# Kernel tuning notes

Measured on AMD Instinct MI355X. Metric: run time of the kernel, lower is better.

The kernel has to match this reference:

```python
import jax, jax.numpy as jnp
import numpy as np

B, SEQ, I_TSIZE, H, N_LAYERS = 512, 256, 64, 512, 2
E_CONST = 2.7183


def setup_inputs() -> dict:
    key = jax.random.key(0)
    ks = jax.random.split(key, 16)
    feats = jax.random.normal(ks[0], (B, SEQ, I_TSIZE - 1), dtype=jnp.float32)
    dt = jax.random.uniform(ks[1], (B, SEQ, 1), dtype=jnp.float32)  # elapsed time >= 0
    inputs_t = jnp.concatenate([feats, dt], axis=-1)  # [B, SEQ, I_TSIZE]
    i_size = I_TSIZE - 1
    inp = {"inputs_t": inputs_t}
    in_dims = [i_size, H]
    for l in range(N_LAYERS):
        c_inp = in_dims[l]
        s = 1.0 / np.sqrt(c_inp + H)
        inp[f"W{l}"] = jax.random.normal(ks[2 + 4 * l], (4 * H, c_inp + H), dtype=jnp.float32) * s
        inp[f"b{l}"] = jax.random.normal(ks[3 + 4 * l], (4 * H,), dtype=jnp.float32) * s
        sd = 1.0 / np.sqrt(H)
        inp[f"Wd{l}"] = jax.random.normal(ks[4 + 4 * l], (H, H), dtype=jnp.float32) * sd
        inp[f"bd{l}"] = jax.random.normal(ks[5 + 4 * l], (H,), dtype=jnp.float32) * sd
    return inp


def _tlstm_layer(curr_inp, W, b, Wd, bd):
    # curr_inp: [B, SEQ, feat+1] (last channel = dt). Scan over REVERSED time,
    # as in the torch loop `for t_seq in reversed(range(seq_l))`.
    batch = curr_inp.shape[0]
    h0 = jnp.zeros((batch, H), dtype=curr_inp.dtype)
    c0 = jnp.zeros((batch, H), dtype=curr_inp.dtype)

    def step(carry, xt):
        h, c = carry
        x, dt = xt[:, :-1], xt[:, -1:]
        T = 1.0 / jnp.log(dt + E_CONST)          # [B,1], broadcasts over H
        C_ST = jnp.tanh(h @ Wd.T + bd)
        h = h - C_ST + T * C_ST                  # time-decay correction
        z = jnp.concatenate([x, h], axis=1) @ W.T + b  # [B, 4H]
        ci, cf, co, cg = jnp.split(z, 4, axis=1)
        c_next = jax.nn.sigmoid(cf) * c + jax.nn.sigmoid(ci) * jnp.tanh(cg)
        h_next = jax.nn.sigmoid(co) * jnp.tanh(c_next)
        return (h_next, c_next), h_next

    xs = jnp.swapaxes(curr_inp[:, ::-1, :], 0, 1)  # [SEQ, B, feat+1], reversed time
    (h, c), hs = jax.lax.scan(step, (h0, c0), xs)
    # hs is in reversed-time order, matching torch's stack of output_inner
    layer_out = jnp.swapaxes(hs, 0, 1)  # [B, SEQ, H]
    return h, layer_out


def reference(inputs_t, W0, b0, Wd0, bd0, W1, b1, Wd1, bd1):
    t = inputs_t[..., -1:]  # [B, SEQ, 1], forward time order (as in torch code)
    params = [(W0, b0, Wd0, bd0), (W1, b1, Wd1, bd1)]
    curr = inputs_t
    h = None
    for (W, b, Wd, bd) in params:
        h, layer_out = _tlstm_layer(curr, W, b, Wd, bd)
        # NOTE: layer_out is in reversed time order but t is forward order;
        # this faithfully reproduces the original module's concatenation.
        curr = jnp.concatenate([layer_out, t], axis=-1)
    return h
```

## Files before the change

### kernel.cpp

```cpp
#include <hip/hip_runtime.h>
#include <stdint.h>

#define B_    512
#define SEQ_  256
#define H_    512
#define NSEQH (SEQ_ * H_)
#define NBLK  256
#define NTHR  (NBLK * 256)

using f32x4 = __attribute__((ext_vector_type(4))) float;
using s16x8 = __attribute__((ext_vector_type(8))) short;

#define WAITVM(N) asm volatile("s_waitcnt vmcnt(" #N ")" ::: "memory")
#define SBAR()    asm volatile("s_barrier" ::: "memory")

__device__ inline unsigned short f2bf(float f) {
  union { float f; uint32_t u; } x; x.f = f;
  uint32_t u = x.u;
  uint32_t r = u + 0x7fffu + ((u >> 16) & 1u);
  return (unsigned short)(r >> 16);
}
__device__ inline float bf2f(unsigned short h) {
  union { float f; uint32_t u; } x; x.u = ((uint32_t)h) << 16;
  return x.f;
}
__device__ inline float h2f(unsigned short u) {
  _Float16 h; __builtin_memcpy(&h, &u, 2); return (float)h;
}
__device__ inline unsigned short f2h(float f) {
  _Float16 h = (_Float16)f; unsigned short u; __builtin_memcpy(&u, &h, 2); return u;
}
__device__ inline float sigf(float x) { return 1.0f / (1.0f + expf(-x)); }

__device__ inline void gload16(const void* g, void* l) {
  __builtin_amdgcn_global_load_lds(
      (const __attribute__((address_space(1))) void*)g,
      (__attribute__((address_space(3))) void*)l, 16, 0, 0);
}
__device__ inline void gload16c(const void* g, void* l) {
  __builtin_amdgcn_global_load_lds(
      (const __attribute__((address_space(1))) void*)g,
      (__attribute__((address_space(3))) void*)l, 16, 0, 17);
}

__device__ __forceinline__ unsigned short ldh_coh(const unsigned short* p) {
  return __hip_atomic_load(p, __ATOMIC_RELAXED, __HIP_MEMORY_SCOPE_SYSTEM);
}
__device__ __forceinline__ void sth_coh(short* p, unsigned short v) {
  __hip_atomic_store((unsigned short*)p, v, __ATOMIC_RELAXED, __HIP_MEMORY_SCOPE_SYSTEM);
}

__device__ __forceinline__ void gbar_heavy(unsigned* bar) {
  __syncthreads();
  if (threadIdx.x == 0) {
    unsigned g = __hip_atomic_load(bar + 1, __ATOMIC_RELAXED, __HIP_MEMORY_SCOPE_AGENT);
    unsigned a = __hip_atomic_fetch_add(bar, 1u, __ATOMIC_ACQ_REL, __HIP_MEMORY_SCOPE_AGENT);
    if (a == (unsigned)(NBLK - 1)) {
      __hip_atomic_store(bar, 0u, __ATOMIC_RELAXED, __HIP_MEMORY_SCOPE_AGENT);
      __hip_atomic_store(bar + 1, g + 1u, __ATOMIC_RELEASE, __HIP_MEMORY_SCOPE_AGENT);
    } else {
      while (__hip_atomic_load(bar + 1, __ATOMIC_ACQUIRE, __HIP_MEMORY_SCOPE_AGENT) == g)
        __builtin_amdgcn_s_sleep(2);
    }
  }
  __syncthreads();
}

__device__ __forceinline__ void lbar(unsigned* bar, int& nb) {
  __syncthreads();
  ++nb;
  if (threadIdx.x == 0) {
    unsigned* leaf = bar + 32 + (blockIdx.x >> 5) * 32;
    unsigned* root = bar + 8;
    unsigned old = __hip_atomic_fetch_add(leaf, 1u, __ATOMIC_RELAXED, __HIP_MEMORY_SCOPE_SYSTEM);
    if ((old & 31u) == 31u)
      __hip_atomic_fetch_add(root, 1u, __ATOMIC_RELAXED, __HIP_MEMORY_SCOPE_SYSTEM);
    const unsigned target = (unsigned)(8 * nb);
    while ((int)(__hip_atomic_load(root, __ATOMIC_RELAXED, __HIP_MEMORY_SCOPE_SYSTEM) - target) < 0)
      __builtin_amdgcn_s_sleep(1);
  }
  __syncthreads();
}

__global__ void fill_kernel(float* __restrict__ out, int n, float v) {
  int i = blockIdx.x * blockDim.x + threadIdx.x;
  if (i < n) out[i] = v;
}

__device__ int compute_slot(const int* xcdmap, int myblk) {
  int cnt[8] = {0,0,0,0,0,0,0,0};
  int rank = -1;
  for (int b = 0; b < NBLK; ++b) {
    int x = xcdmap[b] & 7;
    int r = cnt[x]++;
    if (b == myblk) rank = r;
  }
  int myx = xcdmap[myblk] & 7;
  if (rank < 32) return myx * 32 + rank;
  int spill_idx = 0;
  {
    int c2[8] = {0,0,0,0,0,0,0,0};
    for (int b = 0; b < myblk; ++b) {
      int x = xcdmap[b] & 7;
      if (c2[x]++ >= 32) ++spill_idx;
    }
  }
  int k = 0;
  for (int g = 0; g < 8; ++g) {
    int filled = cnt[g] < 32 ? cnt[g] : 32;
    for (int rr = filled; rr < 32; ++rr) {
      if (k == spill_idx) return g * 32 + rr;
      ++k;
    }
  }
  return 0;
}

template<bool CVT>
__device__ __forceinline__ void g1_phase(
    char* LDS, int m0, int n0,
    const short* hhi, const short* hlo,
    const short* Wds, const float* bd, const float* tm1,
    short* huhi, short* hulo,
    const unsigned short* lo0_t, short* xhhi, short* xhlo)
{
  const int tid = threadIdx.x;
  const int w = tid >> 6, l = tid & 63;
  const int sr = tid >> 3;
  const int scs = (tid & 7) ^ (sr & 7);

  auto stage = [&](int kt) {
    char* base = LDS + (kt & 3) * 16384;
    const int kb = kt << 6;
    const size_t aoff = (size_t)(m0 + sr) * H_ + kb + scs * 8;
    gload16c(hhi + aoff, base + w * 1024);
    gload16c(hlo + aoff, base + 4096 + w * 1024);
    const size_t boff = (size_t)(n0 + sr) * 1024 + kb + scs * 8;
    gload16(Wds + boff,       base + 8192  + w * 1024);
    gload16(Wds + boff + 512, base + 12288 + w * 1024);
  };

  stage(0); stage(1); stage(2);

  const int wm = w & 1, wn = w >> 1;
  const int ar = wm * 16 + (l & 15);
  const int br = wn * 16 + (l & 15);
  const int koff = (l >> 4) * 16;
  const int aswz = (ar & 7) << 4;
  const int bswz = (br & 7) << 4;

  f32x4 acc = {0.f, 0.f, 0.f, 0.f};

  for (int kt = 0; kt < 8; ++kt) {
    if (kt < 6)       WAITVM(8);
    else if (kt == 6) WAITVM(4);
    else              WAITVM(0);
    SBAR();
    if (kt + 3 < 8) stage(kt + 3);
    char* base = LDS + (kt & 3) * 16384;
#pragma unroll
    for (int k2 = 0; k2 < 2; ++k2) {
      const int ao = (ar * 128 + k2 * 64 + koff) ^ aswz;
      const int bo = (br * 128 + k2 * 64 + koff) ^ bswz;
      s16x8 a_hi = *(const s16x8*)(base + ao);
      s16x8 a_lo = *(const s16x8*)(base + 4096 + ao);
      s16x8 b_hi = *(const s16x8*)(base + 8192 + bo);
      s16x8 b_lo = *(const s16x8*)(base + 12288 + bo);
      acc = __builtin_amdgcn_mfma_f32_16x16x32_bf16(a_hi, b_hi, acc, 0, 0, 0);
      acc = __builtin_amdgcn_mfma_f32_16x16x32_bf16(a_lo, b_hi, acc, 0, 0, 0);
      acc = __builtin_amdgcn_mfma_f32_16x16x32_bf16(a_hi, b_lo, acc, 0, 0, 0);
    }
  }

  const int n_abs = n0 + wn * 16 + (l & 15);
  const int mbase = m0 + wm * 16 + (l >> 4) * 4;
  const float bv = bd[n_abs];
#pragma unroll
  for (int r = 0; r < 4; ++r) {
    const int m_abs = mbase + r;
    const size_t off = (size_t)m_abs * H_ + n_abs;
    float cst = tanhf(acc[r] + bv);
    float hv = bf2f(ldh_coh((const unsigned short*)hhi + off)) +
               bf2f(ldh_coh((const unsigned short*)hlo + off));
    float hu = hv + tm1[m_abs] * cst;
    unsigned short hi = f2bf(hu);
    sth_coh(huhi + off, hi);
    sth_coh(hulo + off, f2bf(hu - bf2f(hi)));
    if (CVT) {
      float xv = h2f(ldh_coh(lo0_t + (size_t)m_abs * NSEQH + n_abs));
      unsigned short xh = f2bf(xv);
      sth_coh(xhhi + off, xh);
      sth_coh(xhlo + off, f2bf(xv - bf2f(xh)));
    }
  }
}

template<int K, int XK, int XSTR, bool STORE_LO0, bool XCOH>
__device__ __forceinline__ void g2_phase(
    char* LDS, int m0, int j0,
    const short* xhi, const short* xlo,
    const short* huhi, const short* hulo,
    const short* Wsp, const float* bias,
    f32x4& cv, short* hhi, short* hlo,
    unsigned short* lo0_t)
{
  constexpr int NT = K / 64;
  constexpr int KPS = 2 * K;
  const int tid = threadIdx.x;
  const int w = tid >> 6, l = tid & 63;

  auto stage = [&](int kt) {
    char* base = LDS + (kt & 1) * 32768;
    const int kb = kt << 6;
#pragma unroll
    for (int j = 0; j < 2; ++j) {
      const int s = tid + j * 256;
      const int r = s >> 3;
      const int cs = (s & 7) ^ (r & 7);
      const int dst = j * 4096 + w * 1024;
      if (kb < XK) {
        const size_t aoff = (size_t)(m0 + r) * XSTR + kb + cs * 8;
        if (XCOH) { gload16c(xhi + aoff, base + dst); gload16c(xlo + aoff, base + 8192 + dst); }
        else      { gload16 (xhi + aoff, base + dst); gload16 (xlo + aoff, base + 8192 + dst); }
      } else {
        const size_t aoff = (size_t)(m0 + r) * H_ + (kb - XK) + cs * 8;
        gload16c(huhi + aoff, base + dst);
        gload16c(hulo + aoff, base + 8192 + dst);
      }
      const int src_n = (r >> 4) * H_ + j0 + (r & 15);
      const size_t boff = (size_t)src_n * KPS + kb + cs * 8;
      gload16(Wsp + boff,     base + 16384 + dst);
      gload16(Wsp + boff + K, base + 24576 + dst);
    }
  };

  stage(0); stage(1);

  const int ar = w * 16 + (l & 15);
  const int koff = (l >> 4) * 16;
  const int aswz = (ar & 7) << 4;

  f32x4 acc[4];
#pragma unroll
  for (int i = 0; i < 4; ++i) acc[i] = (f32x4){0.f, 0.f, 0.f, 0.f};

  for (int kt = 0; kt < NT; ++kt) {
    if (kt + 1 < NT) WAITVM(8);
    else             WAITVM(0);
    SBAR();
    char* base = LDS + (kt & 1) * 32768;
#pragma unroll
    for (int k2 = 0; k2 < 2; ++k2) {
      const int ao = (ar * 128 + k2 * 64 + koff) ^ aswz;
      s16x8 a_hi = *(const s16x8*)(base + ao);
      s16x8 a_lo = *(const s16x8*)(base + 8192 + ao);
#pragma unroll
      for (int nf = 0; nf < 4; ++nf) {
        const int br = nf * 16 + (l & 15);
        const int bo = (br * 128 + k2 * 64 + koff) ^ ((br & 7) << 4);
        s16x8 b_hi = *(const s16x8*)(base + 16384 + bo);
        s16x8 b_lo = *(const s16x8*)(base + 24576 + bo);
        acc[nf] = __builtin_amdgcn_mfma_f32_16x16x32_bf16(a_hi, b_hi, acc[nf], 0, 0, 0);
        acc[nf] = __builtin_amdgcn_mfma_f32_16x16x32_bf16(a_lo, b_hi, acc[nf], 0, 0, 0);
        acc[nf] = __builtin_amdgcn_mfma_f32_16x16x32_bf16(a_hi, b_lo, acc[nf], 0, 0, 0);
      }
    }
    SBAR();
    if (kt + 2 < NT) stage(kt + 2);
  }

  const int j_abs = j0 + (l & 15);
  const float bi  = bias[j_abs];
  const float bfv = bias[H_ + j_abs];
  const float bo  = bias[2 * H_ + j_abs];
  const float bg  = bias[3 * H_ + j_abs];
  const int mbase = m0 + w * 16 + (l >> 4) * 4;
#pragma unroll
  for (int r = 0; r < 4; ++r) {
    const int m_abs = mbase + r;
    float zi = acc[0][r] + bi;
    float zf = acc[1][r] + bfv;
    float zo = acc[2][r] + bo;
    float zg = acc[3][r] + bg;
    float cn = sigf(zf) * cv[r] + sigf(zi) * tanhf(zg);
    float hn = sigf(zo) * tanhf(cn);
    cv[r] = cn;
    const size_t off = (size_t)m_abs * H_ + j_abs;
    unsigned short hi = f2bf(hn);
    sth_coh(hhi + off, hi);
    sth_coh(hlo + off, f2bf(hn - bf2f(hi)));
    if (STORE_LO0)
      sth_coh((short*)(lo0_t + (size_t)m_abs * NSEQH + j_abs), f2h(hn));
  }
}

__global__ __launch_bounds__(256, 1) void persist(
    const float* inputs,
    const float* W0, const float* b0, const float* Wd0, const float* bd0,
    const float* W1, const float* b1, const float* Wd1, const float* bd1,
    float* out,
    unsigned short* lo0, short* xinhi, short* xinlo,
    short* hhi, short* hlo, short* huhi, short* hulo,
    short* xhhi, short* xhlo,
    float* Tm1T, short* Wd0s, short* Wd1s, short* W0s, short* W1s,
    unsigned* bar, int* xcdmap)
{
  __shared__ __align__(16) char LDS[65536];
  const int gtid = blockIdx.x * 256 + threadIdx.x;
  int nb = 0;

  if (threadIdx.x == 0) {
    unsigned xcc;
    asm volatile("s_getreg_b32 %0, hwreg(20, 0, 32)" : "=s"(xcc));
    xcdmap[blockIdx.x] = (int)(xcc & 7u);
  }

  auto dosplit = [&](const float* W, short* Ws, int N, int Ksrc, int Kpad, int pad_at) {
    const int total = N * Kpad;
    for (int idx = gtid; idx < total; idx += NTHR) {
      int n = idx / Kpad, c = idx - n * Kpad;
      int sc = c;
      if (pad_at >= 0) { if (c == pad_at) sc = -1; else if (c > pad_at) sc = c - 1; }
      float v = 0.f;
      if (sc >= 0 && sc < Ksrc) v = W[(size_t)n * Ksrc + sc];
      unsigned short hi = f2bf(v);
      unsigned short lo = f2bf(v - bf2f(hi));
      size_t base = (size_t)n * (2 * Kpad);
      Ws[base + c]        = (short)hi;
      Ws[base + Kpad + c] = (short)lo;
    }
  };
  dosplit(Wd0, Wd0s, 512, 512, 512, -1);
  dosplit(Wd1, Wd1s, 512, 512, 512, -1);
  dosplit(W0, W0s, 2048, 575, 576, 63);
  dosplit(W1, W1s, 2048, 1024, 1024, -1);
  for (int idx = gtid; idx < B_ * SEQ_ * 64; idx += NTHR) {
    float v = inputs[idx];
    unsigned short hi = f2bf(v);
    xinhi[idx] = (short)hi;
    xinlo[idx] = (short)f2bf(v - bf2f(hi));
  }
  for (int idx = gtid; idx < B_ * SEQ_; idx += NTHR) {
    int b = idx / SEQ_, t = idx - b * SEQ_;
    float dt = inputs[(size_t)b * (SEQ_ * 64) + t * 64 + 63];
    Tm1T[t * B_ + b] = 1.0f / logf(dt + 2.7183f) - 1.0f;
  }
  for (int idx = gtid; idx < B_ * H_; idx += NTHR) {
    hhi[idx] = 0; hlo[idx] = 0;
  }
  gbar_heavy(bar);

  const int myw = compute_slot(xcdmap, blockIdx.x);
  const int wg = myw >> 5, rr = myw & 31;
  const int g1_n0 = (wg * 2 + (rr & 1)) * 32;
  const int g1_m0 = (rr >> 1) * 32;
  const int g2_j0 = (wg * 4 + (rr & 3)) * 16;
  const int g2_m0 = (rr >> 2) * 64;

  for (int layer = 0; layer < 2; ++layer) {
    f32x4 cv = {0.f, 0.f, 0.f, 0.f};
    if (layer == 1) {
      for (int idx = gtid; idx < B_ * H_; idx += NTHR) {
        sth_coh(hhi + idx, 0); sth_coh(hlo + idx, 0);
      }
      lbar(bar, nb);
    }
    for (int s = 0; s < SEQ_; ++s) {
      const int torig = SEQ_ - 1 - s;
      if (layer == 0) {
        g1_phase<false>(LDS, g1_m0, g1_n0, hhi, hlo, Wd0s, bd0,
                        Tm1T + (size_t)torig * B_, huhi, hulo,
                        nullptr, nullptr, nullptr);
        lbar(bar, nb);
        g2_phase<576, 64, SEQ_ * 64, true, false>(
            LDS, g2_m0, g2_j0,
            xinhi + (size_t)torig * 64, xinlo + (size_t)torig * 64,
            huhi, hulo, W0s, b0, cv, hhi, hlo,
            lo0 + (size_t)s * H_);
        lbar(bar, nb);
      } else {
        g1_phase<true>(LDS, g1_m0, g1_n0, hhi, hlo, Wd1s, bd1,
                       Tm1T + (size_t)torig * B_, huhi, hulo,
                       lo0 + (size_t)torig * H_, xhhi, xhlo);
        lbar(bar, nb);
        g2_phase<1024, 512, H_, false, true>(
            LDS, g2_m0, g2_j0,
            xhhi, xhlo, huhi, hulo, W1s, b1,
            cv, hhi, hlo, nullptr);
        lbar(bar, nb);
      }
    }
  }

  for (int idx = gtid; idx < B_ * H_; idx += NTHR)
    out[idx] = bf2f(ldh_coh((const unsigned short*)hhi + idx)) +
               bf2f(ldh_coh((const unsigned short*)hlo + idx));
}

extern "C" void kernel_launch(void* const* d_in, const int* in_sizes, int n_in,
                              void* d_out, int out_size, void* d_ws, size_t ws_size,
                              hipStream_t stream) {
  const float* inputs = (const float*)d_in[0];
  const float* W0  = (const float*)d_in[1];
  const float* b0  = (const float*)d_in[2];
  const float* Wd0 = (const float*)d_in[3];
  const float* bd0 = (const float*)d_in[4];
  const float* W1  = (const float*)d_in[5];
  const float* b1  = (const float*)d_in[6];
  const float* Wd1 = (const float*)d_in[7];
  const float* bd1 = (const float*)d_in[8];

  char* ws = (char*)d_ws;
  size_t off = 0;
  auto alloc = [&](size_t bytes) -> char* {
    char* p = ws + off;
    off += (bytes + 1023) & ~(size_t)1023;
    return p;
  };
  unsigned* bar = (unsigned*)alloc(2048);
  int* xcdmap = (int*)alloc(NBLK * 4);
  unsigned short* lo0 = (unsigned short*)alloc((size_t)B_ * SEQ_ * H_ * 2);
  short* xinhi = (short*)alloc((size_t)B_ * SEQ_ * 64 * 2);
  short* xinlo = (short*)alloc((size_t)B_ * SEQ_ * 64 * 2);
  short* hhi   = (short*)alloc((size_t)B_ * H_ * 2);
  short* hlo   = (short*)alloc((size_t)B_ * H_ * 2);
  short* huhi  = (short*)alloc((size_t)B_ * H_ * 2);
  short* hulo  = (short*)alloc((size_t)B_ * H_ * 2);
  short* xhhi  = (short*)alloc((size_t)B_ * H_ * 2);
  short* xhlo  = (short*)alloc((size_t)B_ * H_ * 2);
  float* Tm1T  = (float*)alloc((size_t)SEQ_ * B_ * 4);
  short* Wd0s  = (short*)alloc((size_t)512 * 1024 * 2);
  short* Wd1s  = (short*)alloc((size_t)512 * 1024 * 2);
  short* W0s   = (short*)alloc((size_t)2048 * 1152 * 2);
  short* W1s   = (short*)alloc((size_t)2048 * 2048 * 2);

  if (off > ws_size) {
    fill_kernel<<<(out_size + 255) / 256, 256, 0, stream>>>(
        (float*)d_out, out_size, (float)(ws_size >> 20));
    return;
  }

  hipMemsetAsync(bar, 0, 2048, stream);
  persist<<<NBLK, 256, 0, stream>>>(
      inputs, W0, b0, Wd0, bd0, W1, b1, Wd1, bd1,
      (float*)d_out,
      lo0, xinhi, xinlo,
      hhi, hlo, huhi, hulo, xhhi, xhlo,
      Tm1T, Wd0s, Wd1s, W0s, W1s, bar, xcdmap);
}
```

Baseline: 10.31 ms.

## Double persistent block count with half-size blocks and prime weight slices into L2

Runs the persistent kernel as 512 blocks of 128 threads instead of 256 blocks of 256. The XCD slot mapping, barrier targets, per-block GEMM tiles and LDS staging layouts are all rescaled to match. It also adds a prime pass in which one block per column slice reads its Wd and W weight slices so they are cached before the time loop. The goal is to spread the latency-bound recurrent steps over more CUs and warm the caches. The cost is a doubled barrier participant count, more blocks per CU, and extra startup reads.

After: 12.44 ms. 20.6% more time.

```diff
diff --git a/kernel.cpp b/kernel.cpp
--- a/kernel.cpp
+++ b/kernel.cpp
@@ -5,8 +5,9 @@
 #define SEQ_  256
 #define H_    512
 #define NSEQH (SEQ_ * H_)
-#define NBLK  256
-#define NTHR  (NBLK * 256)
+#define NBLK  512
+#define TPB   128
+#define NTHR  (NBLK * TPB)
 
 using f32x4 = __attribute__((ext_vector_type(4))) float;
 using s16x8 = __attribute__((ext_vector_type(8))) short;
@@ -75,7 +76,7 @@
     unsigned old = __hip_atomic_fetch_add(leaf, 1u, __ATOMIC_RELAXED, __HIP_MEMORY_SCOPE_SYSTEM);
     if ((old & 31u) == 31u)
       __hip_atomic_fetch_add(root, 1u, __ATOMIC_RELAXED, __HIP_MEMORY_SCOPE_SYSTEM);
-    const unsigned target = (unsigned)(8 * nb);
+    const unsigned target = (unsigned)(16 * nb);
     while ((int)(__hip_atomic_load(root, __ATOMIC_RELAXED, __HIP_MEMORY_SCOPE_SYSTEM) - target) < 0)
       __builtin_amdgcn_s_sleep(1);
   }
@@ -96,20 +97,20 @@
     if (b == myblk) rank = r;
   }
   int myx = xcdmap[myblk] & 7;
-  if (rank < 32) return myx * 32 + rank;
+  if (rank < 64) return myx * 64 + rank;
   int spill_idx = 0;
   {
     int c2[8] = {0,0,0,0,0,0,0,0};
     for (int b = 0; b < myblk; ++b) {
       int x = xcdmap[b] & 7;
-      if (c2[x]++ >= 32) ++spill_idx;
+      if (c2[x]++ >= 64) ++spill_idx;
     }
   }
   int k = 0;
   for (int g = 0; g < 8; ++g) {
-    int filled = cnt[g] < 32 ? cnt[g] : 32;
-    for (int rr = filled; rr < 32; ++rr) {
-      if (k == spill_idx) return g * 32 + rr;
+    int filled = cnt[g] < 64 ? cnt[g] : 64;
+    for (int rr = filled; rr < 64; ++rr) {
+      if (k == spill_idx) return g * 64 + rr;
       ++k;
     }
   }
@@ -126,25 +127,32 @@
 {
   const int tid = threadIdx.x;
   const int w = tid >> 6, l = tid & 63;
-  const int sr = tid >> 3;
-  const int scs = (tid & 7) ^ (sr & 7);
 
   auto stage = [&](int kt) {
-    char* base = LDS + (kt & 3) * 16384;
+    char* base = LDS + (kt & 3) * 12288;
     const int kb = kt << 6;
-    const size_t aoff = (size_t)(m0 + sr) * H_ + kb + scs * 8;
-    gload16c(hhi + aoff, base + w * 1024);
-    gload16c(hlo + aoff, base + 4096 + w * 1024);
-    const size_t boff = (size_t)(n0 + sr) * 1024 + kb + scs * 8;
-    gload16(Wds + boff,       base + 8192  + w * 1024);
-    gload16(Wds + boff + 512, base + 12288 + w * 1024);
+#pragma unroll
+    for (int j = 0; j < 2; ++j) {
+      const int s = tid + j * TPB;
+      const int r = s >> 3;
+      const int cs = (s & 7) ^ (r & 7);
+      const size_t aoff = (size_t)(m0 + r) * H_ + kb + cs * 8;
+      gload16c(hhi + aoff, base + j * 2048 + w * 1024);
+      gload16c(hlo + aoff, base + 4096 + j * 2048 + w * 1024);
+    }
+    {
+      const int r = tid >> 3;
+      const int cs = (tid & 7) ^ (r & 7);
+      const size_t boff = (size_t)(n0 + r) * 1024 + kb + cs * 8;
+      gload16(Wds + boff,       base + 8192  + w * 1024);
+      gload16(Wds + boff + 512, base + 10240 + w * 1024);
+    }
   };
 
   stage(0); stage(1); stage(2);
 
-  const int wm = w & 1, wn = w >> 1;
-  const int ar = wm * 16 + (l & 15);
-  const int br = wn * 16 + (l & 15);
+  const int ar = w * 16 + (l & 15);
+  const int br = l & 15;
   const int koff = (l >> 4) * 16;
   const int aswz = (ar & 7) << 4;
   const int bswz = (br & 7) << 4;
@@ -152,12 +160,12 @@
   f32x4 acc = {0.f, 0.f, 0.f, 0.f};
 
   for (int kt = 0; kt < 8; ++kt) {
-    if (kt < 6)       WAITVM(8);
-    else if (kt == 6) WAITVM(4);
+    if (kt < 6)       WAITVM(12);
+    else if (kt == 6) WAITVM(6);
     else              WAITVM(0);
     SBAR();
     if (kt + 3 < 8) stage(kt + 3);
-    char* base = LDS + (kt & 3) * 16384;
+    char* base = LDS + (kt & 3) * 12288;
 #pragma unroll
     for (int k2 = 0; k2 < 2; ++k2) {
       const int ao = (ar * 128 + k2 * 64 + koff) ^ aswz;
@@ -165,15 +173,15 @@
       s16x8 a_hi = *(const s16x8*)(base + ao);
       s16x8 a_lo = *(const s16x8*)(base + 4096 + ao);
       s16x8 b_hi = *(const s16x8*)(base + 8192 + bo);
-      s16x8 b_lo = *(const s16x8*)(base + 12288 + bo);
+      s16x8 b_lo = *(const s16x8*)(base + 10240 + bo);
       acc = __builtin_amdgcn_mfma_f32_16x16x32_bf16(a_hi, b_hi, acc, 0, 0, 0);
       acc = __builtin_amdgcn_mfma_f32_16x16x32_bf16(a_lo, b_hi, acc, 0, 0, 0);
       acc = __builtin_amdgcn_mfma_f32_16x16x32_bf16(a_hi, b_lo, acc, 0, 0, 0);
     }
   }
 
-  const int n_abs = n0 + wn * 16 + (l & 15);
-  const int mbase = m0 + wm * 16 + (l >> 4) * 4;
+  const int n_abs = n0 + (l & 15);
+  const int mbase = m0 + w * 16 + (l >> 4) * 4;
   const float bv = bd[n_abs];
 #pragma unroll
   for (int r = 0; r < 4; ++r) {
@@ -210,27 +218,34 @@
   const int w = tid >> 6, l = tid & 63;
 
   auto stage = [&](int kt) {
-    char* base = LDS + (kt & 1) * 32768;
+    char* base = LDS + (kt & 1) * 24576;
     const int kb = kt << 6;
 #pragma unroll
     for (int j = 0; j < 2; ++j) {
-      const int s = tid + j * 256;
+      const int s = tid + j * TPB;
       const int r = s >> 3;
       const int cs = (s & 7) ^ (r & 7);
-      const int dst = j * 4096 + w * 1024;
+      const int dst = j * 2048 + w * 1024;
       if (kb < XK) {
         const size_t aoff = (size_t)(m0 + r) * XSTR + kb + cs * 8;
-        if (XCOH) { gload16c(xhi + aoff, base + dst); gload16c(xlo + aoff, base + 8192 + dst); }
-        else      { gload16 (xhi + aoff, base + dst); gload16 (xlo + aoff, base + 8192 + dst); }
+        if (XCOH) { gload16c(xhi + aoff, base + dst); gload16c(xlo + aoff, base + 4096 + dst); }
+        else      { gload16 (xhi + aoff, base + dst); gload16 (xlo + aoff, base + 4096 + dst); }
       } else {
         const size_t aoff = (size_t)(m0 + r) * H_ + (kb - XK) + cs * 8;
         gload16c(huhi + aoff, base + dst);
-        gload16c(hulo + aoff, base + 8192 + dst);
+        gload16c(hulo + aoff, base + 4096 + dst);
       }
+    }
+#pragma unroll
+    for (int j = 0; j < 4; ++j) {
+      const int s = tid + j * TPB;
+      const int r = s >> 3;
+      const int cs = (s & 7) ^ (r & 7);
       const int src_n = (r >> 4) * H_ + j0 + (r & 15);
       const size_t boff = (size_t)src_n * KPS + kb + cs * 8;
-      gload16(Wsp + boff,     base + 16384 + dst);
-      gload16(Wsp + boff + K, base + 24576 + dst);
+      const int dst = 8192 + j * 2048 + w * 1024;
+      gload16(Wsp + boff,     base + dst);
+      gload16(Wsp + boff + K, base + 8192 + dst);
     }
   };
 
@@ -245,21 +260,21 @@
   for (int i = 0; i < 4; ++i) acc[i] = (f32x4){0.f, 0.f, 0.f, 0.f};
 
   for (int kt = 0; kt < NT; ++kt) {
-    if (kt + 1 < NT) WAITVM(8);
+    if (kt + 1 < NT) WAITVM(12);
     else             WAITVM(0);
     SBAR();
-    char* base = LDS + (kt & 1) * 32768;
+    char* base = LDS + (kt & 1) * 24576;
 #pragma unroll
     for (int k2 = 0; k2 < 2; ++k2) {
       const int ao = (ar * 128 + k2 * 64 + koff) ^ aswz;
       s16x8 a_hi = *(const s16x8*)(base + ao);
-      s16x8 a_lo = *(const s16x8*)(base + 8192 + ao);
+      s16x8 a_lo = *(const s16x8*)(base + 4096 + ao);
 #pragma unroll
       for (int nf = 0; nf < 4; ++nf) {
         const int br = nf * 16 + (l & 15);
         const int bo = (br * 128 + k2 * 64 + koff) ^ ((br & 7) << 4);
-        s16x8 b_hi = *(const s16x8*)(base + 16384 + bo);
-        s16x8 b_lo = *(const s16x8*)(base + 24576 + bo);
+        s16x8 b_hi = *(const s16x8*)(base + 8192 + bo);
+        s16x8 b_lo = *(const s16x8*)(base + 16384 + bo);
         acc[nf] = __builtin_amdgcn_mfma_f32_16x16x32_bf16(a_hi, b_hi, acc[nf], 0, 0, 0);
         acc[nf] = __builtin_amdgcn_mfma_f32_16x16x32_bf16(a_lo, b_hi, acc[nf], 0, 0, 0);
         acc[nf] = __builtin_amdgcn_mfma_f32_16x16x32_bf16(a_hi, b_lo, acc[nf], 0, 0, 0);
@@ -294,7 +309,7 @@
   }
 }
 
-__global__ __launch_bounds__(256, 1) void persist(
+__global__ __launch_bounds__(TPB, 1) void persist(
     const float* inputs,
     const float* W0, const float* b0, const float* Wd0, const float* bd0,
     const float* W1, const float* b1, const float* Wd1, const float* bd1,
@@ -303,10 +318,11 @@
     short* hhi, short* hlo, short* huhi, short* hulo,
     short* xhhi, short* xhlo,
     float* Tm1T, short* Wd0s, short* Wd1s, short* W0s, short* W1s,
-    unsigned* bar, int* xcdmap)
+    unsigned* bar, int* xcdmap, float* sink)
 {
-  __shared__ __align__(16) char LDS[65536];
-  const int gtid = blockIdx.x * 256 + threadIdx.x;
+  __shared__ __align__(16) char LDS[49152];
+  const int gtid = blockIdx.x * TPB + threadIdx.x;
+  const int tid = threadIdx.x;
   int nb = 0;
 
   if (threadIdx.x == 0) {
@@ -351,11 +367,26 @@
   gbar_heavy(bar);
 
   const int myw = compute_slot(xcdmap, blockIdx.x);
-  const int wg = myw >> 5, rr = myw & 31;
-  const int g1_n0 = (wg * 2 + (rr & 1)) * 32;
-  const int g1_m0 = (rr >> 1) * 32;
-  const int g2_j0 = (wg * 4 + (rr & 3)) * 16;
-  const int g2_m0 = (rr >> 2) * 64;
+  const int wg = myw >> 6, rr = myw & 63;
+  const int sl = wg * 4 + (rr & 3);
+  const int g1_n0 = sl * 16;
+  const int g1_m0 = (rr >> 2) * 32;
+  const int g2_j0 = sl * 16;
+  const int g2_m0 = (rr >> 2) * 32;
+
+  auto prime = [&](const short* p, int nshorts) {
+    float a = 0.f;
+    for (int i = tid * 8; i + 8 <= nshorts; i += TPB * 8) {
+      f32x4 v = *(const f32x4*)(p + i);
+      a += v[0] + v[1] + v[2] + v[3];
+    }
+    if (a == 1.0e38f) *sink = a;
+  };
+  if ((rr >> 2) == 0) {
+    prime(Wd0s + g1_n0 * 1024, 16 * 1024);
+    for (int g = 0; g < 4; ++g)
+      prime(W0s + (size_t)(g * 512 + g2_j0) * 2304, 16 * 2304);
+  }
 
   for (int layer = 0; layer < 2; ++layer) {
     f32x4 cv = {0.f, 0.f, 0.f, 0.f};
@@ -364,6 +395,11 @@
         sth_coh(hhi + idx, 0); sth_coh(hlo + idx, 0);
       }
       lbar(bar, nb);
+      if ((rr >> 2) == 0) {
+        prime(Wd1s + g1_n0 * 1024, 16 * 1024);
+        for (int g = 0; g < 4; ++g)
+          prime(W1s + (size_t)(g * 512 + g2_j0) * 4096, 16 * 4096);
+      }
     }
     for (int s = 0; s < SEQ_; ++s) {
       const int torig = SEQ_ - 1 - s;
@@ -417,8 +453,9 @@
     off += (bytes + 1023) & ~(size_t)1023;
     return p;
   };
-  unsigned* bar = (unsigned*)alloc(2048);
+  unsigned* bar = (unsigned*)alloc(4096);
   int* xcdmap = (int*)alloc(NBLK * 4);
+  float* sink = (float*)alloc(1024);
   unsigned short* lo0 = (unsigned short*)alloc((size_t)B_ * SEQ_ * H_ * 2);
   short* xinhi = (short*)alloc((size_t)B_ * SEQ_ * 64 * 2);
   short* xinlo = (short*)alloc((size_t)B_ * SEQ_ * 64 * 2);
@@ -440,11 +477,11 @@
     return;
   }
 
-  hipMemsetAsync(bar, 0, 2048, stream);
-  persist<<<NBLK, 256, 0, stream>>>(
+  hipMemsetAsync(bar, 0, 4096, stream);
+  persist<<<NBLK, TPB, 0, stream>>>(
       inputs, W0, b0, Wd0, bd0, W1, b1, Wd1, bd1,
       (float*)d_out,
       lo0, xinhi, xinlo,
       hhi, hlo, huhi, hulo, xhhi, xhlo,
-      Tm1T, Wd0s, Wd1s, W0s, W1s, bar, xcdmap);
-}
+      Tm1T, Wd0s, Wd1s, W0s, W1s, bar, xcdmap, sink);
+}
```

## Replace grid barriers with per-batch-tile flags and deepen GEMM pipelines

Applied to the files above, without the earlier changes.

Remaps work so that the g1 and g2 phases of each 64-row batch tile are owned by the same 32 blocks. The two grid-wide barriers per timestep become per-tile counter flags, so tiles advance independently and do not wait on the whole grid. The g2 GEMM moves from a double-buffered to a 4-stage LDS pipeline, dropping the second barrier per k-tile, and g1 is retiled. LDS is raised to 128KB of dynamic shared memory, which risks occupancy and adds the correctness burden of the new flag protocol.

Measured after the change: 16.43 ms. +59.4%, slower.

```diff
diff --git a/kernel.cpp b/kernel.cpp
--- a/kernel.cpp
+++ b/kernel.cpp
@@ -82,6 +82,20 @@
   __syncthreads();
 }
 
+__device__ __forceinline__ void flag_signal(unsigned* f) {
+  WAITVM(0);
+  __syncthreads();
+  if (threadIdx.x == 0)
+    __hip_atomic_fetch_add(f, 1u, __ATOMIC_RELAXED, __HIP_MEMORY_SCOPE_SYSTEM);
+}
+__device__ __forceinline__ void flag_wait(unsigned* f, unsigned target) {
+  if (threadIdx.x == 0 && target) {
+    while (__hip_atomic_load(f, __ATOMIC_RELAXED, __HIP_MEMORY_SCOPE_SYSTEM) < target)
+      __builtin_amdgcn_s_sleep(1);
+  }
+  __syncthreads();
+}
+
 __global__ void fill_kernel(float* __restrict__ out, int n, float v) {
   int i = blockIdx.x * blockDim.x + threadIdx.x;
   if (i < n) out[i] = v;
@@ -126,45 +140,48 @@
 {
   const int tid = threadIdx.x;
   const int w = tid >> 6, l = tid & 63;
-  const int sr = tid >> 3;
-  const int scs = (tid & 7) ^ (sr & 7);
+  const int ar_ = (tid & 127) >> 3;
+  const int acs = (tid & 7) ^ (ar_ & 7);
+  const short* Asel = (tid < 128) ? hhi : hlo;
+  const int adst = ((tid < 128) ? 0 : 2048) + (w & 1) * 1024;
 
   auto stage = [&](int kt) {
-    char* base = LDS + (kt & 3) * 16384;
+    char* base = LDS + (kt & 3) * 20480;
     const int kb = kt << 6;
-    const size_t aoff = (size_t)(m0 + sr) * H_ + kb + scs * 8;
-    gload16c(hhi + aoff, base + w * 1024);
-    gload16c(hlo + aoff, base + 4096 + w * 1024);
-    const size_t boff = (size_t)(n0 + sr) * 1024 + kb + scs * 8;
-    gload16(Wds + boff,       base + 8192  + w * 1024);
-    gload16(Wds + boff + 512, base + 12288 + w * 1024);
+    gload16c(Asel + (size_t)(m0 + ar_) * H_ + kb + acs * 8, base + adst);
+#pragma unroll
+    for (int q = 0; q < 4; ++q) {
+      const int r = ((q & 1) << 5) + w * 8 + (l >> 3);
+      const int cs = (l & 7) ^ (r & 7);
+      gload16(Wds + (size_t)(n0 + r) * 1024 + kb + ((q >> 1) ? 512 : 0) + cs * 8,
+              base + 4096 + (q >> 1) * 8192 + (q & 1) * 4096 + w * 1024);
+    }
   };
 
   stage(0); stage(1); stage(2);
 
-  const int wm = w & 1, wn = w >> 1;
-  const int ar = wm * 16 + (l & 15);
-  const int br = wn * 16 + (l & 15);
+  const int row_a = l & 15;
+  const int swz_a = (row_a & 7) << 4;
+  const int br = w * 16 + (l & 15);
+  const int swz_b = (br & 7) << 4;
   const int koff = (l >> 4) * 16;
-  const int aswz = (ar & 7) << 4;
-  const int bswz = (br & 7) << 4;
 
   f32x4 acc = {0.f, 0.f, 0.f, 0.f};
 
   for (int kt = 0; kt < 8; ++kt) {
-    if (kt < 6)       WAITVM(8);
-    else if (kt == 6) WAITVM(4);
+    if (kt < 6)       WAITVM(10);
+    else if (kt == 6) WAITVM(5);
     else              WAITVM(0);
     SBAR();
     if (kt + 3 < 8) stage(kt + 3);
-    char* base = LDS + (kt & 3) * 16384;
+    char* base = LDS + (kt & 3) * 20480;
 #pragma unroll
     for (int k2 = 0; k2 < 2; ++k2) {
-      const int ao = (ar * 128 + k2 * 64 + koff) ^ aswz;
-      const int bo = (br * 128 + k2 * 64 + koff) ^ bswz;
+      const int ao = (row_a * 128 + k2 * 64 + koff) ^ swz_a;
+      const int bo = (br * 128 + k2 * 64 + koff) ^ swz_b;
       s16x8 a_hi = *(const s16x8*)(base + ao);
-      s16x8 a_lo = *(const s16x8*)(base + 4096 + ao);
-      s16x8 b_hi = *(const s16x8*)(base + 8192 + bo);
+      s16x8 a_lo = *(const s16x8*)(base + 2048 + ao);
+      s16x8 b_hi = *(const s16x8*)(base + 4096 + bo);
       s16x8 b_lo = *(const s16x8*)(base + 12288 + bo);
       acc = __builtin_amdgcn_mfma_f32_16x16x32_bf16(a_hi, b_hi, acc, 0, 0, 0);
       acc = __builtin_amdgcn_mfma_f32_16x16x32_bf16(a_lo, b_hi, acc, 0, 0, 0);
@@ -172,8 +189,8 @@
     }
   }
 
-  const int n_abs = n0 + wn * 16 + (l & 15);
-  const int mbase = m0 + wm * 16 + (l >> 4) * 4;
+  const int n_abs = n0 + w * 16 + (l & 15);
+  const int mbase = m0 + (l >> 4) * 4;
   const float bv = bd[n_abs];
 #pragma unroll
   for (int r = 0; r < 4; ++r) {
@@ -210,48 +227,57 @@
   const int w = tid >> 6, l = tid & 63;
 
   auto stage = [&](int kt) {
-    char* base = LDS + (kt & 1) * 32768;
+    char* base = LDS + (kt & 3) * 32768;
     const int kb = kt << 6;
 #pragma unroll
-    for (int j = 0; j < 2; ++j) {
-      const int s = tid + j * 256;
-      const int r = s >> 3;
-      const int cs = (s & 7) ^ (r & 7);
-      const int dst = j * 4096 + w * 1024;
+    for (int q = 0; q < 4; ++q) {
+      const bool hi = q < 2;
+      const int qq = q & 1;
+      const int r = qq * 32 + w * 8 + (l >> 3);
+      const int cs = (l & 7) ^ (r & 7);
+      char* dst = base + (hi ? 0 : 8192) + qq * 4096 + w * 1024;
       if (kb < XK) {
+        const short* asrc = hi ? xhi : xlo;
         const size_t aoff = (size_t)(m0 + r) * XSTR + kb + cs * 8;
-        if (XCOH) { gload16c(xhi + aoff, base + dst); gload16c(xlo + aoff, base + 8192 + dst); }
-        else      { gload16 (xhi + aoff, base + dst); gload16 (xlo + aoff, base + 8192 + dst); }
+        if (XCOH) gload16c(asrc + aoff, dst);
+        else      gload16 (asrc + aoff, dst);
       } else {
-        const size_t aoff = (size_t)(m0 + r) * H_ + (kb - XK) + cs * 8;
-        gload16c(huhi + aoff, base + dst);
-        gload16c(hulo + aoff, base + 8192 + dst);
+        const short* asrc = hi ? huhi : hulo;
+        gload16c(asrc + (size_t)(m0 + r) * H_ + (kb - XK) + cs * 8, dst);
       }
+    }
+#pragma unroll
+    for (int q = 0; q < 4; ++q) {
+      const bool hi = q < 2;
+      const int qq = q & 1;
+      const int r = qq * 32 + w * 8 + (l >> 3);
+      const int cs = (l & 7) ^ (r & 7);
       const int src_n = (r >> 4) * H_ + j0 + (r & 15);
-      const size_t boff = (size_t)src_n * KPS + kb + cs * 8;
-      gload16(Wsp + boff,     base + 16384 + dst);
-      gload16(Wsp + boff + K, base + 24576 + dst);
+      gload16(Wsp + (size_t)src_n * KPS + kb + (hi ? 0 : K) + cs * 8,
+              base + 16384 + (hi ? 0 : 8192) + qq * 4096 + w * 1024);
     }
   };
 
-  stage(0); stage(1);
+  stage(0); stage(1); stage(2);
 
   const int ar = w * 16 + (l & 15);
+  const int swz_a = (ar & 7) << 4;
   const int koff = (l >> 4) * 16;
-  const int aswz = (ar & 7) << 4;
 
   f32x4 acc[4];
 #pragma unroll
   for (int i = 0; i < 4; ++i) acc[i] = (f32x4){0.f, 0.f, 0.f, 0.f};
 
   for (int kt = 0; kt < NT; ++kt) {
-    if (kt + 1 < NT) WAITVM(8);
-    else             WAITVM(0);
+    if (kt < NT - 2)       WAITVM(16);
+    else if (kt == NT - 2) WAITVM(8);
+    else                   WAITVM(0);
     SBAR();
-    char* base = LDS + (kt & 1) * 32768;
+    if (kt + 3 < NT) stage(kt + 3);
+    char* base = LDS + (kt & 3) * 32768;
 #pragma unroll
     for (int k2 = 0; k2 < 2; ++k2) {
-      const int ao = (ar * 128 + k2 * 64 + koff) ^ aswz;
+      const int ao = (ar * 128 + k2 * 64 + koff) ^ swz_a;
       s16x8 a_hi = *(const s16x8*)(base + ao);
       s16x8 a_lo = *(const s16x8*)(base + 8192 + ao);
 #pragma unroll
@@ -265,8 +291,6 @@
         acc[nf] = __builtin_amdgcn_mfma_f32_16x16x32_bf16(a_hi, b_lo, acc[nf], 0, 0, 0);
       }
     }
-    SBAR();
-    if (kt + 2 < NT) stage(kt + 2);
   }
 
   const int j_abs = j0 + (l & 15);
@@ -305,7 +329,7 @@
     float* Tm1T, short* Wd0s, short* Wd1s, short* W0s, short* W1s,
     unsigned* bar, int* xcdmap)
 {
-  __shared__ __align__(16) char LDS[65536];
+  extern __shared__ __align__(16) char LDS[];
   const int gtid = blockIdx.x * 256 + threadIdx.x;
   int nb = 0;
 
@@ -352,46 +376,54 @@
 
   const int myw = compute_slot(xcdmap, blockIdx.x);
   const int wg = myw >> 5, rr = myw & 31;
-  const int g1_n0 = (wg * 2 + (rr & 1)) * 32;
-  const int g1_m0 = (rr >> 1) * 32;
-  const int g2_j0 = (wg * 4 + (rr & 3)) * 16;
-  const int g2_m0 = (rr >> 2) * 64;
+  const int t = rr >> 2;
+  const int c = wg * 4 + (rr & 3);
+  const int g1_m0 = t * 64 + (c >> 3) * 16;
+  const int g1_n0 = (c & 7) * 64;
+  const int g2_m0 = t * 64;
+  const int g2_j0 = c * 16;
+  unsigned* g1d = bar + 512 + t * 16;
+  unsigned* g2d = bar + 768 + t * 16;
 
   for (int layer = 0; layer < 2; ++layer) {
     f32x4 cv = {0.f, 0.f, 0.f, 0.f};
     if (layer == 1) {
+      lbar(bar, nb);
       for (int idx = gtid; idx < B_ * H_; idx += NTHR) {
         sth_coh(hhi + idx, 0); sth_coh(hlo + idx, 0);
       }
       lbar(bar, nb);
     }
     for (int s = 0; s < SEQ_; ++s) {
+      const int ss = layer * SEQ_ + s;
       const int torig = SEQ_ - 1 - s;
-      if (layer == 0) {
+      flag_wait(g2d, 32u * (unsigned)ss);
+      if (layer == 0)
         g1_phase<false>(LDS, g1_m0, g1_n0, hhi, hlo, Wd0s, bd0,
                         Tm1T + (size_t)torig * B_, huhi, hulo,
                         nullptr, nullptr, nullptr);
-        lbar(bar, nb);
+      else
+        g1_phase<true>(LDS, g1_m0, g1_n0, hhi, hlo, Wd1s, bd1,
+                       Tm1T + (size_t)torig * B_, huhi, hulo,
+                       lo0 + (size_t)torig * H_, xhhi, xhlo);
+      flag_signal(g1d);
+      flag_wait(g1d, 32u * (unsigned)(ss + 1));
+      if (layer == 0)
         g2_phase<576, 64, SEQ_ * 64, true, false>(
             LDS, g2_m0, g2_j0,
             xinhi + (size_t)torig * 64, xinlo + (size_t)torig * 64,
             huhi, hulo, W0s, b0, cv, hhi, hlo,
             lo0 + (size_t)s * H_);
-        lbar(bar, nb);
-      } else {
-        g1_phase<true>(LDS, g1_m0, g1_n0, hhi, hlo, Wd1s, bd1,
-                       Tm1T + (size_t)torig * B_, huhi, hulo,
-                       lo0 + (size_t)torig * H_, xhhi, xhlo);
-        lbar(bar, nb);
+      else
         g2_phase<1024, 512, H_, false, true>(
             LDS, g2_m0, g2_j0,
             xhhi, xhlo, huhi, hulo, W1s, b1,
             cv, hhi, hlo, nullptr);
-        lbar(bar, nb);
-      }
-    }
-  }
-
+      flag_signal(g2d);
+    }
+  }
+
+  lbar(bar, nb);
   for (int idx = gtid; idx < B_ * H_; idx += NTHR)
     out[idx] = bf2f(ldh_coh((const unsigned short*)hhi + idx)) +
                bf2f(ldh_coh((const unsigned short*)hlo + idx));
@@ -417,7 +449,7 @@
     off += (bytes + 1023) & ~(size_t)1023;
     return p;
   };
-  unsigned* bar = (unsigned*)alloc(2048);
+  unsigned* bar = (unsigned*)alloc(4096);
   int* xcdmap = (int*)alloc(NBLK * 4);
   unsigned short* lo0 = (unsigned short*)alloc((size_t)B_ * SEQ_ * H_ * 2);
   short* xinhi = (short*)alloc((size_t)B_ * SEQ_ * 64 * 2);
@@ -440,8 +472,11 @@
     return;
   }
 
-  hipMemsetAsync(bar, 0, 2048, stream);
-  persist<<<NBLK, 256, 0, stream>>>(
+  hipFuncSetAttribute(reinterpret_cast<const void*>(&persist),
+                      hipFuncAttributeMaxDynamicSharedMemorySize, 131072);
+
+  hipMemsetAsync(bar, 0, 4096, stream);
+  persist<<<NBLK, 256, 131072, stream>>>(
       inputs, W0, b0, Wd0, bd0, W1, b1, Wd1, bd1,
       (float*)d_out,
       lo0, xinhi, xinlo,
```

## Load weights via registers and triple-buffer LDS in recurrent GEMM phases

Applied to the files above, without the earlier changes.

Weight tiles in both GEMM phases are now fetched into VGPRs with plain global loads and written to LDS one stage later, while activations still use direct global-to-LDS DMA. The LDS ring moves from 2–4 buffers to 3 buffers, backed by 96KB of dynamic shared memory. This lets the trailing barrier in g2 be dropped, so each K-step needs a single barrier and weight fetches overlap compute further ahead. In exchange it uses more registers and LDS, removes forceinline from both phases, and relies on exact waitcnt accounting that now also drains lgkmcnt.

After: 14.77 ms. +43.2%, slower.

```diff
diff --git a/kernel.cpp b/kernel.cpp
--- a/kernel.cpp
+++ b/kernel.cpp
@@ -11,7 +11,7 @@
 using f32x4 = __attribute__((ext_vector_type(4))) float;
 using s16x8 = __attribute__((ext_vector_type(8))) short;
 
-#define WAITVM(N) asm volatile("s_waitcnt vmcnt(" #N ")" ::: "memory")
+#define WAITVL(N) asm volatile("s_waitcnt vmcnt(" #N ") lgkmcnt(0)" ::: "memory")
 #define SBAR()    asm volatile("s_barrier" ::: "memory")
 
 __device__ inline unsigned short f2bf(float f) {
@@ -32,7 +32,7 @@
 }
 __device__ inline float sigf(float x) { return 1.0f / (1.0f + expf(-x)); }
 
-__device__ inline void gload16(const void* g, void* l) {
+__device__ inline void gldsw(const void* g, void* l) {
   __builtin_amdgcn_global_load_lds(
       (const __attribute__((address_space(1))) void*)g,
       (__attribute__((address_space(3))) void*)l, 16, 0, 0);
@@ -41,6 +41,11 @@
   __builtin_amdgcn_global_load_lds(
       (const __attribute__((address_space(1))) void*)g,
       (__attribute__((address_space(3))) void*)l, 16, 0, 17);
+}
+
+__device__ __forceinline__ void wload(const short* p, s16x8& d) {
+  asm volatile("global_load_dwordx4 %0, %1, off"
+               : "=&v"(d) : "v"((unsigned long long)p));
 }
 
 __device__ __forceinline__ unsigned short ldh_coh(const unsigned short* p) {
@@ -117,7 +122,7 @@
 }
 
 template<bool CVT>
-__device__ __forceinline__ void g1_phase(
+__device__ void g1_phase(
     char* LDS, int m0, int n0,
     const short* hhi, const short* hlo,
     const short* Wds, const float* bd, const float* tm1,
@@ -128,19 +133,33 @@
   const int w = tid >> 6, l = tid & 63;
   const int sr = tid >> 3;
   const int scs = (tid & 7) ^ (sr & 7);
-
-  auto stage = [&](int kt) {
-    char* base = LDS + (kt & 3) * 16384;
-    const int kb = kt << 6;
-    const size_t aoff = (size_t)(m0 + sr) * H_ + kb + scs * 8;
+  const int wc = tid & 7;
+  const int wdst = (sr * 128 + wc * 16) ^ ((sr & 7) << 4);
+
+  s16x8 vwh, vwl;
+  s16x8 twh, twl;
+
+  auto wloadW = [&](int kt, s16x8& a, s16x8& b) {
+    const short* p = Wds + (size_t)(n0 + sr) * 1024 + (kt << 6) + wc * 8;
+    wload(p, a); wload(p + 512, b);
+  };
+  auto dswriteW = [&](int kt, s16x8& a, s16x8& b) {
+    char* base = LDS + (kt % 3) * 16384;
+    *(s16x8*)(base + 8192 + wdst) = a;
+    *(s16x8*)(base + 12288 + wdst) = b;
+  };
+  auto admaA = [&](int kt) {
+    char* base = LDS + (kt % 3) * 16384;
+    const size_t aoff = (size_t)(m0 + sr) * H_ + (kt << 6) + scs * 8;
     gload16c(hhi + aoff, base + w * 1024);
     gload16c(hlo + aoff, base + 4096 + w * 1024);
-    const size_t boff = (size_t)(n0 + sr) * 1024 + kb + scs * 8;
-    gload16(Wds + boff,       base + 8192  + w * 1024);
-    gload16(Wds + boff + 512, base + 12288 + w * 1024);
-  };
-
-  stage(0); stage(1); stage(2);
+  };
+
+  wloadW(0, vwh, vwl); wloadW(1, twh, twl);
+  WAITVL(0);
+  dswriteW(0, vwh, vwl); dswriteW(1, twh, twl);
+  wloadW(2, vwh, vwl);
+  admaA(0); admaA(1);
 
   const int wm = w & 1, wn = w >> 1;
   const int ar = wm * 16 + (l & 15);
@@ -152,12 +171,13 @@
   f32x4 acc = {0.f, 0.f, 0.f, 0.f};
 
   for (int kt = 0; kt < 8; ++kt) {
-    if (kt < 6)       WAITVM(8);
-    else if (kt == 6) WAITVM(4);
-    else              WAITVM(0);
+    if (kt < 7) WAITVL(2);
+    else        WAITVL(0);
     SBAR();
-    if (kt + 3 < 8) stage(kt + 3);
-    char* base = LDS + (kt & 3) * 16384;
+    if (kt + 2 < 8) dswriteW(kt + 2, vwh, vwl);
+    if (kt + 3 < 8) wloadW(kt + 3, vwh, vwl);
+    if (kt + 2 < 8) admaA(kt + 2);
+    char* base = LDS + (kt % 3) * 16384;
 #pragma unroll
     for (int k2 = 0; k2 < 2; ++k2) {
       const int ao = (ar * 128 + k2 * 64 + koff) ^ aswz;
@@ -196,7 +216,7 @@
 }
 
 template<int K, int XK, int XSTR, bool STORE_LO0, bool XCOH>
-__device__ __forceinline__ void g2_phase(
+__device__ void g2_phase(
     char* LDS, int m0, int j0,
     const short* xhi, const short* xlo,
     const short* huhi, const short* hulo,
@@ -209,49 +229,77 @@
   const int tid = threadIdx.x;
   const int w = tid >> 6, l = tid & 63;
 
-  auto stage = [&](int kt) {
-    char* base = LDS + (kt & 1) * 32768;
+  const int wr0 = tid >> 3, wc0 = tid & 7;
+  const int wr1 = wr0 + 32;
+  const int wd0 = (wr0 * 128 + wc0 * 16) ^ ((wr0 & 7) << 4);
+  const int wd1 = (wr1 * 128 + wc0 * 16) ^ ((wr1 & 7) << 4);
+  const int srcn0 = (wr0 >> 4) * H_ + j0 + (wr0 & 15);
+  const int srcn1 = (wr1 >> 4) * H_ + j0 + (wr1 & 15);
+
+  s16x8 vh0, vh1, vl0, vl1;
+  s16x8 th0, th1, tl0, tl1;
+
+  auto wloadW = [&](int kt, s16x8& a0, s16x8& a1, s16x8& b0, s16x8& b1) {
+    const int kb = kt << 6;
+    const short* p0 = Wsp + (size_t)srcn0 * KPS + kb + wc0 * 8;
+    const short* p1 = Wsp + (size_t)srcn1 * KPS + kb + wc0 * 8;
+    wload(p0, a0); wload(p1, a1);
+    wload(p0 + K, b0); wload(p1 + K, b1);
+  };
+  auto dswriteW = [&](int kt, s16x8& a0, s16x8& a1, s16x8& b0, s16x8& b1) {
+    char* base = LDS + (kt % 3) * 32768;
+    *(s16x8*)(base + 16384 + wd0) = a0;
+    *(s16x8*)(base + 16384 + wd1) = a1;
+    *(s16x8*)(base + 24576 + wd0) = b0;
+    *(s16x8*)(base + 24576 + wd1) = b1;
+  };
+  auto admaA = [&](int kt) {
+    char* base = LDS + (kt % 3) * 32768;
     const int kb = kt << 6;
 #pragma unroll
     for (int j = 0; j < 2; ++j) {
       const int s = tid + j * 256;
       const int r = s >> 3;
       const int cs = (s & 7) ^ (r & 7);
-      const int dst = j * 4096 + w * 1024;
+      char* dhi = base + j * 4096 + w * 1024;
+      char* dlo = base + 8192 + j * 4096 + w * 1024;
       if (kb < XK) {
         const size_t aoff = (size_t)(m0 + r) * XSTR + kb + cs * 8;
-        if (XCOH) { gload16c(xhi + aoff, base + dst); gload16c(xlo + aoff, base + 8192 + dst); }
-        else      { gload16 (xhi + aoff, base + dst); gload16 (xlo + aoff, base + 8192 + dst); }
+        if (XCOH) { gload16c(xhi + aoff, dhi); gload16c(xlo + aoff, dlo); }
+        else      { gldsw(xhi + aoff, dhi);    gldsw(xlo + aoff, dlo); }
       } else {
         const size_t aoff = (size_t)(m0 + r) * H_ + (kb - XK) + cs * 8;
-        gload16c(huhi + aoff, base + dst);
-        gload16c(hulo + aoff, base + 8192 + dst);
+        gload16c(huhi + aoff, dhi);
+        gload16c(hulo + aoff, dlo);
       }
-      const int src_n = (r >> 4) * H_ + j0 + (r & 15);
-      const size_t boff = (size_t)src_n * KPS + kb + cs * 8;
-      gload16(Wsp + boff,     base + 16384 + dst);
-      gload16(Wsp + boff + K, base + 24576 + dst);
-    }
-  };
-
-  stage(0); stage(1);
+    }
+  };
+
+  wloadW(0, vh0, vh1, vl0, vl1); wloadW(1, th0, th1, tl0, tl1);
+  WAITVL(0);
+  dswriteW(0, vh0, vh1, vl0, vl1); dswriteW(1, th0, th1, tl0, tl1);
+  wloadW(2, vh0, vh1, vl0, vl1);
+  admaA(0); admaA(1);
 
   const int ar = w * 16 + (l & 15);
+  const int swz_a = (ar & 7) << 4;
   const int koff = (l >> 4) * 16;
-  const int aswz = (ar & 7) << 4;
 
   f32x4 acc[4];
 #pragma unroll
   for (int i = 0; i < 4; ++i) acc[i] = (f32x4){0.f, 0.f, 0.f, 0.f};
 
   for (int kt = 0; kt < NT; ++kt) {
-    if (kt + 1 < NT) WAITVM(8);
-    else             WAITVM(0);
+    if (kt < NT - 1) WAITVL(4);
+    else             WAITVL(0);
     SBAR();
-    char* base = LDS + (kt & 1) * 32768;
+    if (kt + 2 < NT) dswriteW(kt + 2, vh0, vh1, vl0, vl1);
+    if (kt + 3 < NT) wloadW(kt + 3, vh0, vh1, vl0, vl1);
+    if (kt + 2 < NT) admaA(kt + 2);
+    char* base = LDS + (kt % 3) * 32768;
 #pragma unroll
     for (int k2 = 0; k2 < 2; ++k2) {
-      const int ao = (ar * 128 + k2 * 64 + koff) ^ aswz;
+      const int ao = (ar * 128 + k2 * 64 + koff) ^ swz_a;
       s16x8 a_hi = *(const s16x8*)(base + ao);
       s16x8 a_lo = *(const s16x8*)(base + 8192 + ao);
 #pragma unroll
@@ -265,8 +313,6 @@
         acc[nf] = __builtin_amdgcn_mfma_f32_16x16x32_bf16(a_hi, b_lo, acc[nf], 0, 0, 0);
       }
     }
-    SBAR();
-    if (kt + 2 < NT) stage(kt + 2);
   }
 
   const int j_abs = j0 + (l & 15);
@@ -305,7 +351,7 @@
     float* Tm1T, short* Wd0s, short* Wd1s, short* W0s, short* W1s,
     unsigned* bar, int* xcdmap)
 {
-  __shared__ __align__(16) char LDS[65536];
+  extern __shared__ __align__(16) char LDS[];
   const int gtid = blockIdx.x * 256 + threadIdx.x;
   int nb = 0;
 
@@ -417,7 +463,7 @@
     off += (bytes + 1023) & ~(size_t)1023;
     return p;
   };
-  unsigned* bar = (unsigned*)alloc(2048);
+  unsigned* bar = (unsigned*)alloc(4096);
   int* xcdmap = (int*)alloc(NBLK * 4);
   unsigned short* lo0 = (unsigned short*)alloc((size_t)B_ * SEQ_ * H_ * 2);
   short* xinhi = (short*)alloc((size_t)B_ * SEQ_ * 64 * 2);
@@ -440,8 +486,11 @@
     return;
   }
 
-  hipMemsetAsync(bar, 0, 2048, stream);
-  persist<<<NBLK, 256, 0, stream>>>(
+  hipFuncSetAttribute(reinterpret_cast<const void*>(&persist),
+                      hipFuncAttributeMaxDynamicSharedMemorySize, 131072);
+
+  hipMemsetAsync(bar, 0, 4096, stream);
+  persist<<<NBLK, 256, 98304, stream>>>(
       inputs, W0, b0, Wd0, bd0, W1, b1, Wd1, bd1,
       (float*)d_out,
       lo0, xinhi, xinlo,
```
